# Kernel tuning notes

Measured on AMD Instinct MI355X. Metric: run time of the kernel, lower is better.

The kernel has to match this reference:

```python
import jax, jax.numpy as jnp
import numpy as np

N_NODES = 100000
N_EDGES = 1600000
D_IN, D_HID, D_OUT = 64, 128, 64


def setup_inputs() -> dict:
    key = jax.random.key(0)
    ks = jax.random.split(key, 12)
    s = lambda d: 1.0 / np.sqrt(d)
    return {
        "x": jax.random.normal(ks[0], (N_NODES, D_IN), dtype=jnp.float32),
        "edge_index": jax.random.randint(ks[1], (2, N_EDGES), 0, N_NODES, dtype=jnp.int64),
        # conv1 MLP: Linear(D_IN->D_HID), ReLU, Linear(D_HID->D_HID)
        "W1a": jax.random.uniform(ks[2], (D_IN, D_HID), jnp.float32, -s(D_IN), s(D_IN)),
        "b1a": jnp.zeros((D_HID,), jnp.float32),
        "W1b": jax.random.uniform(ks[3], (D_HID, D_HID), jnp.float32, -s(D_HID), s(D_HID)),
        "b1b": jnp.zeros((D_HID,), jnp.float32),
        # conv2 MLP: Linear(D_HID->D_HID), ReLU, Linear(D_HID->D_HID)
        "W2a": jax.random.uniform(ks[4], (D_HID, D_HID), jnp.float32, -s(D_HID), s(D_HID)),
        "b2a": jnp.zeros((D_HID,), jnp.float32),
        "W2b": jax.random.uniform(ks[5], (D_HID, D_HID), jnp.float32, -s(D_HID), s(D_HID)),
        "b2b": jnp.zeros((D_HID,), jnp.float32),
        # final projection Linear(D_HID->D_OUT)
        "Wlin": jax.random.uniform(ks[6], (D_HID, D_OUT), jnp.float32, -s(D_HID), s(D_HID)),
        "blin": jnp.zeros((D_OUT,), jnp.float32),
    }


def _gin_conv(h, src, dst, Wa, ba, Wb, bb, num_nodes):
    # GINConv (eps=0): MLP((1+eps)*x + sum_{j->i} x_j)
    agg = jax.ops.segment_sum(h[src], dst, num_segments=num_nodes)  # [N, d]
    z = h + agg
    z = jax.nn.relu(z @ Wa + ba)
    return z @ Wb + bb


def reference(x, edge_index, W1a, b1a, W1b, b1b, W2a, b2a, W2b, b2b, Wlin, blin):
    n = x.shape[0]
    src, dst = edge_index[0], edge_index[1]
    h = jax.nn.relu(_gin_conv(x, src, dst, W1a, b1a, W1b, b1b, n))
    h = jax.nn.relu(_gin_conv(h, src, dst, W2a, b2a, W2b, b2b, n))
    return h @ Wlin + blin  # [N, D_OUT]
```

## Files before the change

kernel.cpp:

```cpp
#include <hip/hip_runtime.h>
#include <hip/hip_fp16.h>


typedef __attribute__((ext_vector_type(8))) short short8;
typedef __attribute__((ext_vector_type(4))) float f32x4;
union F8 { unsigned u[4]; short8 s; };

__device__ inline unsigned bfpair(float v) {
    unsigned u = __float_as_uint(v);
    unsigned rh = u + 0x7fffu + ((u >> 16) & 1u);
    unsigned hf = rh & 0xffff0000u;
    float lof = v - __uint_as_float(hf);
    unsigned ul = __float_as_uint(lof);
    unsigned rl = ul + 0x7fffu + ((ul >> 16) & 1u);
    return (rh >> 16) | (rl & 0xffff0000u);
}


constexpr int BUCKET_SHIFT = 9;
constexpr int BUCKET_NODES = 1 << BUCKET_SHIFT;
constexpr int CAP = 10240;
constexpr int EPB = 4096;
constexpr int NBUCK_MAX = 256;

__global__ __launch_bounds__(256) void init_gcur_kernel(int* __restrict__ gcur, int nbuck) {
    int i = threadIdx.x;
    if (i < nbuck) gcur[i] = i * CAP;
}

__global__ __launch_bounds__(256) void bucket_scatter_kernel(const int* __restrict__ ei, int E,
                                                             int* __restrict__ gcur,
                                                             int* __restrict__ gpk,
                                                             int nbuck) {
    __shared__ int spk[EPB];
    __shared__ unsigned char sbuck[EPB];
    __shared__ int lcnt[NBUCK_MAX];
    __shared__ int lbase[NBUCK_MAX];
    __shared__ int lcur[NBUCK_MAX];
    __shared__ int gbase[NBUCK_MAX];
    __shared__ int stmp[256];

    const int t = threadIdx.x;
    const int e0 = blockIdx.x * EPB;
    const int ecnt = min(EPB, E - e0);

    for (int i = t; i < NBUCK_MAX; i += 256) lcnt[i] = 0;
    __syncthreads();

    for (int i = t; i < ecnt; i += 256) {
        int d = ei[E + e0 + i];
        atomicAdd(&lcnt[d >> BUCKET_SHIFT], 1);
    }
    __syncthreads();

    int v = lcnt[t];
    stmp[t] = v;
    __syncthreads();
    #pragma unroll
    for (int off = 1; off < 256; off <<= 1) {
        int add = (t >= off) ? stmp[t - off] : 0;
        __syncthreads();
        stmp[t] += add;
        __syncthreads();
    }
    lbase[t] = stmp[t] - v;
    lcur[t] = stmp[t] - v;
    __syncthreads();

    for (int i = t; i < ecnt; i += 256) {
        int s = ei[e0 + i];
        int d = ei[E + e0 + i];
        int b = d >> BUCKET_SHIFT;
        int p = atomicAdd(&lcur[b], 1);
        spk[p] = ((d & (BUCKET_NODES - 1)) << 17) | s;
        sbuck[p] = (unsigned char)b;
    }
    __syncthreads();

    if (t < nbuck) {
        int c = lcnt[t];
        gbase[t] = (c > 0) ? atomicAdd(&gcur[t], c) : 0;
    }
    __syncthreads();

    for (int i = t; i < ecnt; i += 256) {
        int b = sbuck[i];
        int gp = gbase[b] + (i - lbase[b]);
        if (gp < (b + 1) * CAP) gpk[gp] = spk[i];
    }
}

__global__ __launch_bounds__(256) void bucket_hist_kernel(const int* __restrict__ gpk,
                                                          const int* __restrict__ gcur,
                                                          int* __restrict__ cnt, int N) {
    __shared__ int h[BUCKET_NODES];
    const int t = threadIdx.x;
    const int b = blockIdx.x;
    const int base = b << BUCKET_SHIFT;
    for (int i = t; i < BUCKET_NODES; i += 256) h[i] = 0;
    __syncthreads();
    int cb = min(gcur[b] - b * CAP, CAP);
    const int* pp = gpk + (size_t)b * CAP;
    for (int i = t; i < cb; i += 256) atomicAdd(&h[((unsigned)pp[i]) >> 17], 1);
    __syncthreads();
    for (int i = t; i < BUCKET_NODES && base + i < N; i += 256) cnt[base + i] = h[i];
}

__global__ __launch_bounds__(256) void scan_block_kernel(const int* __restrict__ cnt,
                                                         int* __restrict__ rs,
                                                         int* __restrict__ partials,
                                                         int N) {
    __shared__ int s[256];
    int t = threadIdx.x;
    int i = blockIdx.x * 256 + t;
    int v = (i < N) ? cnt[i] : 0;
    s[t] = v;
    __syncthreads();
    #pragma unroll
    for (int off = 1; off < 256; off <<= 1) {
        int add = (t >= off) ? s[t - off] : 0;
        __syncthreads();
        s[t] += add;
        __syncthreads();
    }
    if (i < N) rs[i] = s[t] - v;
    if (t == 255) partials[blockIdx.x] = s[255];
}

__global__ __launch_bounds__(512) void scan_partials_kernel(int* __restrict__ partials,
                                                            int nb) {
    __shared__ int s[512];
    int t = threadIdx.x;
    int v = (t < nb) ? partials[t] : 0;
    s[t] = v;
    __syncthreads();
    #pragma unroll
    for (int off = 1; off < 512; off <<= 1) {
        int add = (t >= off) ? s[t - off] : 0;
        __syncthreads();
        s[t] += add;
        __syncthreads();
    }
    if (t < nb) partials[t] = s[t] - v;
}

__global__ __launch_bounds__(256) void scan_add_kernel(int* __restrict__ rs,
                                                       const int* __restrict__ partials,
                                                       int N, int E) {
    int i = blockIdx.x * 256 + threadIdx.x;
    if (i < N) rs[i] += partials[blockIdx.x];
    if (i == 0) rs[N] = E;
}

__global__ __launch_bounds__(256) void bucket_fill_kernel(const int* __restrict__ gpk,
                                                          const int* __restrict__ gcur,
                                                          const int* __restrict__ rs,
                                                          int* __restrict__ edge_src, int N) {
    __shared__ int cur[BUCKET_NODES];
    const int t = threadIdx.x;
    const int b = blockIdx.x;
    const int base = b << BUCKET_SHIFT;
    for (int i = t; i < BUCKET_NODES; i += 256) cur[i] = rs[min(base + i, N)];
    __syncthreads();
    int cb = min(gcur[b] - b * CAP, CAP);
    const int* pp = gpk + (size_t)b * CAP;
    for (int i = t; i < cb; i += 256) {
        unsigned pw = (unsigned)pp[i];
        int p = atomicAdd(&cur[pw >> 17], 1);
        edge_src[p] = (int)(pw & 0x1FFFFu);
    }
}


__global__ __launch_bounds__(256) void convert_fp16_kernel(const float* __restrict__ src,
                                                           __half2* __restrict__ dst, int n2) {
    int i = blockIdx.x * 256 + threadIdx.x;
    if (i < n2) {
        float2 v = reinterpret_cast<const float2*>(src)[i];
        dst[i] = __floats2half2_rn(v.x, v.y);
    }
}

__global__ __launch_bounds__(256) void agg128_fp16(const __half2* __restrict__ H16,
                                                   const int* __restrict__ row_start,
                                                   const int* __restrict__ edge_src,
                                                   __half2* __restrict__ Z16, int N) {
    int wave = threadIdx.x >> 6, lane = threadIdx.x & 63;
    int node = blockIdx.x * 4 + wave;
    if (node >= N) return;
    int beg = row_start[node], end = row_start[node + 1];
    float2 self = __half22float2(H16[(size_t)node * 64 + lane]);
    float a0 = self.x, a1 = self.y;
    int i = beg;
    for (; i + 4 <= end; i += 4) {
        int s0 = edge_src[i], s1 = edge_src[i + 1];
        int s2 = edge_src[i + 2], s3 = edge_src[i + 3];
        float2 v0 = __half22float2(H16[(size_t)s0 * 64 + lane]);
        float2 v1 = __half22float2(H16[(size_t)s1 * 64 + lane]);
        float2 v2 = __half22float2(H16[(size_t)s2 * 64 + lane]);
        float2 v3 = __half22float2(H16[(size_t)s3 * 64 + lane]);
        a0 += (v0.x + v1.x) + (v2.x + v3.x);
        a1 += (v0.y + v1.y) + (v2.y + v3.y);
    }
    for (; i < end; ++i) {
        float2 v = __half22float2(H16[(size_t)edge_src[i] * 64 + lane]);
        a0 += v.x;
        a1 += v.y;
    }
    Z16[(size_t)node * 64 + lane] = __floats2half2_rn(a0, a1);
}

__global__ __launch_bounds__(256) void agg64_fp16(const __half2* __restrict__ H16,
                                                  const int* __restrict__ row_start,
                                                  const int* __restrict__ edge_src,
                                                  __half2* __restrict__ Z16, int N) {
    int t = threadIdx.x;
    int grp = t >> 5;
    int gl = t & 31;
    int node = blockIdx.x * 8 + grp;
    if (node >= N) return;
    int beg = row_start[node], end = row_start[node + 1];
    float2 self = __half22float2(H16[(size_t)node * 32 + gl]);
    float a0 = self.x, a1 = self.y;
    int i = beg;
    for (; i + 4 <= end; i += 4) {
        int s0 = edge_src[i], s1 = edge_src[i + 1];
        int s2 = edge_src[i + 2], s3 = edge_src[i + 3];
        float2 v0 = __half22float2(H16[(size_t)s0 * 32 + gl]);
        float2 v1 = __half22float2(H16[(size_t)s1 * 32 + gl]);
        float2 v2 = __half22float2(H16[(size_t)s2 * 32 + gl]);
        float2 v3 = __half22float2(H16[(size_t)s3 * 32 + gl]);
        a0 += (v0.x + v1.x) + (v2.x + v3.x);
        a1 += (v0.y + v1.y) + (v2.y + v3.y);
    }
    for (; i < end; ++i) {
        float2 v = __half22float2(H16[(size_t)edge_src[i] * 32 + gl]);
        a0 += v.x;
        a1 += v.y;
    }
    Z16[(size_t)node * 32 + gl] = __floats2half2_rn(a0, a1);
}


__global__ __launch_bounds__(256) void prep_weights_kernel(const float* __restrict__ W1a,
                                                           const float* __restrict__ W1b,
                                                           const float* __restrict__ W2a,
                                                           const float* __restrict__ W2b,
                                                           const float* __restrict__ Wlin,
                                                           short* __restrict__ hi,
                                                           short* __restrict__ lo) {
    int i = blockIdx.x * 256 + threadIdx.x;
    const float* W;
    int base, K, N;
    if (i < 8192)       { W = W1a;  base = 0;     K = 64;  N = 128; }
    else if (i < 24576) { W = W1b;  base = 8192;  K = 128; N = 128; }
    else if (i < 40960) { W = W2a;  base = 24576; K = 128; N = 128; }
    else if (i < 57344) { W = W2b;  base = 40960; K = 128; N = 128; }
    else                { W = Wlin; base = 57344; K = 128; N = 64;  }
    int rel = i - base;
    int NT = N >> 4;
    int j  = rel & 7;
    int l  = (rel >> 3) & 63;
    int tc = rel >> 9;
    int nt = tc % NT;
    int c  = tc / NT;
    int n  = nt * 16 + (l & 15);
    int k  = c * 32 + ((l >> 4) << 3) + j;
    float v = W[k * N + n];
    unsigned p = bfpair(v);
    hi[i] = (short)(p & 0xffffu);
    lo[i] = (short)(p >> 16);
}


template <int K>
__device__ inline void stage_global16(const __half2* __restrict__ z, int M, int m0,
                                      unsigned* __restrict__ P, int t) {
    constexpr int KC = K / 32;
    constexpr int NF = 8 * KC * 64;
    #pragma unroll
    for (int fi = t; fi < NF; fi += 256) {
        int l = fi & 63;
        int tc = fi >> 6;
        int c = tc & (KC - 1);
        int T = tc / KC;
        int row = m0 + T * 16 + (l & 15);
        if (row >= M) row = M - 1;
        int kb = c * 32 + ((l >> 4) << 3);
        const __half2* p = z + (size_t)row * (K / 2) + (kb >> 1);
        uint4 v = *reinterpret_cast<const uint4*>(p);
        float2 f0 = __half22float2(*reinterpret_cast<__half2*>(&v.x));
        float2 f1 = __half22float2(*reinterpret_cast<__half2*>(&v.y));
        float2 f2 = __half22float2(*reinterpret_cast<__half2*>(&v.z));
        float2 f3 = __half22float2(*reinterpret_cast<__half2*>(&v.w));
        int base = ((T * KC + c) * 8) * 66 + l;
        P[base + 0 * 66] = bfpair(f0.x);
        P[base + 1 * 66] = bfpair(f0.y);
        P[base + 2 * 66] = bfpair(f1.x);
        P[base + 3 * 66] = bfpair(f1.y);
        P[base + 4 * 66] = bfpair(f2.x);
        P[base + 5 * 66] = bfpair(f2.y);
        P[base + 6 * 66] = bfpair(f3.x);
        P[base + 7 * 66] = bfpair(f3.y);
    }
}

template <int K, int NT>
__device__ inline void stage_compute(const unsigned* __restrict__ P,
                                     const short* __restrict__ WH,
                                     const short* __restrict__ WL,
                                     int w, int lane, f32x4 (*acc)[8]) {
    constexpr int KC = K / 32;
    const short8* bhp = reinterpret_cast<const short8*>(WH) + lane;
    const short8* blp = reinterpret_cast<const short8*>(WL) + lane;
    for (int c = 0; c < KC; ++c) {
        F8 bh[NT], bl[NT];
        #pragma unroll
        for (int nt = 0; nt < NT; ++nt) {
            bh[nt].s = bhp[(c * NT + nt) * 64];
            bl[nt].s = blp[(c * NT + nt) * 64];
        }
        #pragma unroll
        for (int mt = 0; mt < 2; ++mt) {
            const int T = w * 2 + mt;
            const unsigned* Pb = P + ((T * KC + c) * 8) * 66 + lane;
            unsigned d[8];
            #pragma unroll
            for (int j = 0; j < 8; ++j) d[j] = Pb[j * 66];
            F8 ah, al;
            #pragma unroll
            for (int j = 0; j < 4; ++j) {
                ah.u[j] = __builtin_amdgcn_perm(d[2 * j + 1], d[2 * j], 0x05040100u);
                al.u[j] = __builtin_amdgcn_perm(d[2 * j + 1], d[2 * j], 0x07060302u);
            }
            #pragma unroll
            for (int nt = 0; nt < NT; ++nt) {
                acc[mt][nt] = __builtin_amdgcn_mfma_f32_16x16x32_bf16(ah.s, bh[nt].s, acc[mt][nt], 0, 0, 0);
                acc[mt][nt] = __builtin_amdgcn_mfma_f32_16x16x32_bf16(al.s, bh[nt].s, acc[mt][nt], 0, 0, 0);
                acc[mt][nt] = __builtin_amdgcn_mfma_f32_16x16x32_bf16(ah.s, bl[nt].s, acc[mt][nt], 0, 0, 0);
            }
        }
    }
}

__device__ inline void epilogue_tile(const f32x4* acc, const float* __restrict__ bias,
                                     unsigned* __restrict__ Pout, int T, int lane) {
    int q = lane >> 4, ln = lane & 15;
    #pragma unroll
    for (int nt = 0; nt < 8; ++nt) {
        int col = nt * 16 + ln;
        float b = bias[col];
        int c = col >> 5, jj = col & 7, q2 = (col >> 3) & 3;
        int pb = ((T * 4 + c) * 8 + jj) * 66;
        #pragma unroll
        for (int r = 0; r < 4; ++r) {
            float v = fmaxf(acc[nt][r] + b, 0.f);
            Pout[pb + ((q * 4 + r) | (q2 << 4))] = bfpair(v);
        }
    }
}

__global__ __launch_bounds__(256, 2) void mfma_mlp_A(const __half2* __restrict__ z16,
                                                     const short* __restrict__ WaH,
                                                     const short* __restrict__ WaL,
                                                     const float* __restrict__ ba,
                                                     const short* __restrict__ WbH,
                                                     const short* __restrict__ WbL,
                                                     const float* __restrict__ bb,
                                                     __half* __restrict__ H16out, int M) {
    __shared__ unsigned P[8 * 4 * 8 * 66];
    const int t = threadIdx.x;
    const int w = t >> 6, lane = t & 63;
    const int m0 = blockIdx.x * 128;
    const int q = lane >> 4, ln = lane & 15;

    stage_global16<64>(z16, M, m0, P, t);
    __syncthreads();

    f32x4 acc[2][8];
    #pragma unroll
    for (int mt = 0; mt < 2; ++mt)
        #pragma unroll
        for (int i = 0; i < 8; ++i) acc[mt][i] = (f32x4){0.f, 0.f, 0.f, 0.f};
    stage_compute<64, 8>(P, WaH, WaL, w, lane, acc);
    __syncthreads();
    epilogue_tile(acc[0], ba, P, w * 2 + 0, lane);
    epilogue_tile(acc[1], ba, P, w * 2 + 1, lane);
    __syncthreads();

    #pragma unroll
    for (int mt = 0; mt < 2; ++mt)
        #pragma unroll
        for (int i = 0; i < 8; ++i) acc[mt][i] = (f32x4){0.f, 0.f, 0.f, 0.f};
    stage_compute<128, 8>(P, WbH, WbL, w, lane, acc);

    #pragma unroll
    for (int mt = 0; mt < 2; ++mt) {
        #pragma unroll
        for (int nt = 0; nt < 8; ++nt) {
            int col = nt * 16 + ln;
            float b = bb[col];
            #pragma unroll
            for (int r = 0; r < 4; ++r) {
                int row = m0 + (w * 2 + mt) * 16 + q * 4 + r;
                if (row < M) {
                    float v = fmaxf(acc[mt][nt][r] + b, 0.f);
                    H16out[(size_t)row * 128 + col] = __float2half_rn(v);
                }
            }
        }
    }
}

__global__ __launch_bounds__(256, 2) void mfma_mlp_B(const __half2* __restrict__ z16,
                                                     const short* __restrict__ WaH,
                                                     const short* __restrict__ WaL,
                                                     const float* __restrict__ ba,
                                                     const short* __restrict__ WbH,
                                                     const short* __restrict__ WbL,
                                                     const float* __restrict__ bb,
                                                     const short* __restrict__ WlH,
                                                     const short* __restrict__ WlL,
                                                     const float* __restrict__ bl,
                                                     float* __restrict__ Out, int M) {
    __shared__ unsigned P[8 * 4 * 8 * 66];
    const int t = threadIdx.x;
    const int w = t >> 6, lane = t & 63;
    const int m0 = blockIdx.x * 128;
    const int q = lane >> 4, ln = lane & 15;

    stage_global16<128>(z16, M, m0, P, t);
    __syncthreads();

    f32x4 acc[2][8];
    #pragma unroll
    for (int mt = 0; mt < 2; ++mt)
        #pragma unroll
        for (int i = 0; i < 8; ++i) acc[mt][i] = (f32x4){0.f, 0.f, 0.f, 0.f};
    stage_compute<128, 8>(P, WaH, WaL, w, lane, acc);
    __syncthreads();
    epilogue_tile(acc[0], ba, P, w * 2 + 0, lane);
    epilogue_tile(acc[1], ba, P, w * 2 + 1, lane);
    __syncthreads();

    #pragma unroll
    for (int mt = 0; mt < 2; ++mt)
        #pragma unroll
        for (int i = 0; i < 8; ++i) acc[mt][i] = (f32x4){0.f, 0.f, 0.f, 0.f};
    stage_compute<128, 8>(P, WbH, WbL, w, lane, acc);
    __syncthreads();
    epilogue_tile(acc[0], bb, P, w * 2 + 0, lane);
    epilogue_tile(acc[1], bb, P, w * 2 + 1, lane);
    __syncthreads();

    #pragma unroll
    for (int mt = 0; mt < 2; ++mt)
        #pragma unroll
        for (int i = 0; i < 8; ++i) acc[mt][i] = (f32x4){0.f, 0.f, 0.f, 0.f};
    stage_compute<128, 4>(P, WlH, WlL, w, lane, acc);

    #pragma unroll
    for (int mt = 0; mt < 2; ++mt) {
        #pragma unroll
        for (int nt = 0; nt < 4; ++nt) {
            int col = nt * 16 + ln;
            float b = bl[col];
            #pragma unroll
            for (int r = 0; r < 4; ++r) {
                int row = m0 + (w * 2 + mt) * 16 + q * 4 + r;
                if (row < M) Out[(size_t)row * 64 + col] = acc[mt][nt][r] + b;
            }
        }
    }
}


extern "C" void kernel_launch(void* const* d_in, const int* in_sizes, int n_in,
                              void* d_out, int out_size, void* d_ws, size_t ws_size,
                              hipStream_t stream) {
    const float* x    = (const float*)d_in[0];
    const int*   ei   = (const int*)d_in[1];
    const float* W1a  = (const float*)d_in[2];
    const float* b1a  = (const float*)d_in[3];
    const float* W1b  = (const float*)d_in[4];
    const float* b1b  = (const float*)d_in[5];
    const float* W2a  = (const float*)d_in[6];
    const float* b2a  = (const float*)d_in[7];
    const float* W2b  = (const float*)d_in[8];
    const float* b2b  = (const float*)d_in[9];
    const float* Wlin = (const float*)d_in[10];
    const float* blin = (const float*)d_in[11];
    float* out = (float*)d_out;

    const int N = in_sizes[0] / 64;
    const int E = in_sizes[1] / 2;
    const int NBUCK = (N + BUCKET_NODES - 1) >> BUCKET_SHIFT;

    char* ws = (char*)d_ws;
    const size_t bufBytes = (size_t)N * 128 * sizeof(float);
    __half2* Zbuf = (__half2*)(ws + 0);
    char* B = ws + bufBytes;
    size_t off = 3 * bufBytes;
    int* row_start = (int*)(ws + off); off += ((size_t)(N + 1) * 4 + 15) & ~(size_t)15;
    int* cnt       = (int*)(ws + off); off += ((size_t)N * 4 + 15) & ~(size_t)15;
    int* partials  = (int*)(ws + off); off += 4096;
    int* gcur      = (int*)(ws + off); off += 4096;
    int* edge_src  = (int*)(ws + off); off += (size_t)E * 4;
    __half* h116   = (__half*)(ws + off); off += (size_t)N * 128 * 2;
    int* gpk = (int*)B;
    short* wHi = (short*)(B + (32u << 20));
    short* wLo = wHi + 65536;
    __half* x16 = (__half*)(B + (36u << 20));
    short* w1aH = wHi + 0;     short* w1aL = wLo + 0;
    short* w1bH = wHi + 8192;  short* w1bL = wLo + 8192;
    short* w2aH = wHi + 24576; short* w2aL = wLo + 24576;
    short* w2bH = wHi + 40960; short* w2bL = wLo + 40960;
    short* wlH  = wHi + 57344; short* wlL  = wLo + 57344;

    const int NB_N = (N + 255) / 256;
    const int NB_G = (N + 127) / 128;
    const int NB_S = (E + EPB - 1) / EPB;
    const int NB_A128 = (N + 3) / 4;
    const int NB_A64  = (N + 7) / 8;
    const int NB_CVT  = (N * 64 / 2 + 255) / 256;

    prep_weights_kernel<<<256, 256, 0, stream>>>(W1a, W1b, W2a, W2b, Wlin, wHi, wLo);
    convert_fp16_kernel<<<NB_CVT, 256, 0, stream>>>(x, (__half2*)x16, N * 32);

    init_gcur_kernel<<<1, 256, 0, stream>>>(gcur, NBUCK);
    bucket_scatter_kernel<<<NB_S, 256, 0, stream>>>(ei, E, gcur, gpk, NBUCK);
    bucket_hist_kernel<<<NBUCK, 256, 0, stream>>>(gpk, gcur, cnt, N);
    scan_block_kernel<<<NB_N, 256, 0, stream>>>(cnt, row_start, partials, N);
    scan_partials_kernel<<<1, 512, 0, stream>>>(partials, NB_N);
    scan_add_kernel<<<NB_N, 256, 0, stream>>>(row_start, partials, N, E);
    bucket_fill_kernel<<<NBUCK, 256, 0, stream>>>(gpk, gcur, row_start, edge_src, N);

    agg64_fp16<<<NB_A64, 256, 0, stream>>>((const __half2*)x16, row_start, edge_src, Zbuf, N);
    mfma_mlp_A<<<NB_G, 256, 0, stream>>>(Zbuf, w1aH, w1aL, b1a, w1bH, w1bL, b1b, h116, N);

    agg128_fp16<<<NB_A128, 256, 0, stream>>>((const __half2*)h116, row_start, edge_src, Zbuf, N);
    mfma_mlp_B<<<NB_G, 256, 0, stream>>>(Zbuf, w2aH, w2aL, b2a, w2bH, w2bL, b2b,
                                         wlH, wlL, blin, out, N);
}
```

Baseline: 367.8 us.

## Split aggregation feature columns across blocks with 16-lane groups per node

Both neighbor-sum kernels now give each node a 16-lane group that covers only a quarter (128-wide) or half (64-wide) of the feature row. Adjacent blocks handle different column slices of the same 16 nodes. This puts more nodes in flight per wave to hide gather latency. In exchange, every column slice re-reads edge_src and row_start, and each gathered row segment is only 64 bytes, which may lower memory transaction efficiency.

```diff
diff --git a/kernel.cpp b/kernel.cpp
--- a/kernel.cpp
+++ b/kernel.cpp
@@ -181,64 +181,70 @@
     }
 }
 
-__global__ __launch_bounds__(256) void agg128_fp16(const __half2* __restrict__ H16,
-                                                   const int* __restrict__ row_start,
-                                                   const int* __restrict__ edge_src,
-                                                   __half2* __restrict__ Z16, int N) {
-    int wave = threadIdx.x >> 6, lane = threadIdx.x & 63;
-    int node = blockIdx.x * 4 + wave;
+__global__ __launch_bounds__(256) void agg128_fp16_q(const __half2* __restrict__ H16,
+                                                     const int* __restrict__ row_start,
+                                                     const int* __restrict__ edge_src,
+                                                     __half2* __restrict__ Z16, int N) {
+    int b = blockIdx.x;
+    int quarter = b & 3;
+    int grp = threadIdx.x >> 4;
+    int gl = threadIdx.x & 15;
+    int node = (b >> 2) * 16 + grp;
     if (node >= N) return;
+    int co = quarter * 16 + gl;
     int beg = row_start[node], end = row_start[node + 1];
-    float2 self = __half22float2(H16[(size_t)node * 64 + lane]);
+    float2 self = __half22float2(H16[(size_t)node * 64 + co]);
     float a0 = self.x, a1 = self.y;
     int i = beg;
     for (; i + 4 <= end; i += 4) {
         int s0 = edge_src[i], s1 = edge_src[i + 1];
         int s2 = edge_src[i + 2], s3 = edge_src[i + 3];
-        float2 v0 = __half22float2(H16[(size_t)s0 * 64 + lane]);
-        float2 v1 = __half22float2(H16[(size_t)s1 * 64 + lane]);
-        float2 v2 = __half22float2(H16[(size_t)s2 * 64 + lane]);
-        float2 v3 = __half22float2(H16[(size_t)s3 * 64 + lane]);
+        float2 v0 = __half22float2(H16[(size_t)s0 * 64 + co]);
+        float2 v1 = __half22float2(H16[(size_t)s1 * 64 + co]);
+        float2 v2 = __half22float2(H16[(size_t)s2 * 64 + co]);
+        float2 v3 = __half22float2(H16[(size_t)s3 * 64 + co]);
         a0 += (v0.x + v1.x) + (v2.x + v3.x);
         a1 += (v0.y + v1.y) + (v2.y + v3.y);
     }
     for (; i < end; ++i) {
-        float2 v = __half22float2(H16[(size_t)edge_src[i] * 64 + lane]);
+        float2 v = __half22float2(H16[(size_t)edge_src[i] * 64 + co]);
         a0 += v.x;
         a1 += v.y;
     }
-    Z16[(size_t)node * 64 + lane] = __floats2half2_rn(a0, a1);
-}
-
-__global__ __launch_bounds__(256) void agg64_fp16(const __half2* __restrict__ H16,
-                                                  const int* __restrict__ row_start,
-                                                  const int* __restrict__ edge_src,
-                                                  __half2* __restrict__ Z16, int N) {
-    int t = threadIdx.x;
-    int grp = t >> 5;
-    int gl = t & 31;
-    int node = blockIdx.x * 8 + grp;
+    Z16[(size_t)node * 64 + co] = __floats2half2_rn(a0, a1);
+}
+
+__global__ __launch_bounds__(256) void agg64_fp16_h(const __half2* __restrict__ H16,
+                                                    const int* __restrict__ row_start,
+                                                    const int* __restrict__ edge_src,
+                                                    __half2* __restrict__ Z16, int N) {
+    int b = blockIdx.x;
+    int half = b & 1;
+    int grp = threadIdx.x >> 4;
+    int gl = threadIdx.x & 15;
+    int node = (b >> 1) * 16 + grp;
     if (node >= N) return;
+    int co = half * 16 + gl;
     int beg = row_start[node], end = row_start[node + 1];
-    float2 self = __half22float2(H16[(size_t)node * 32 + gl]);
+    float2 self = __half22float2(H16[(size_t)node * 32 + co]);
     float a0 = self.x, a1 = self.y;
     int i = beg;
     for (; i + 4 <= end; i += 4) {
         int s0 = edge_src[i], s1 = edge_src[i + 1];
         int s2 = edge_src[i + 2], s3 = edge_src[i + 3];
-        float2 v0 = __half22float2(H16[(size_t)s0 * 32 + gl]);
-        float2 v1 = __half22float2(H16[(size_t)s1 * 32 + gl]);
-        float2 v2 = __half22float2(H16[(size_t)s2 * 32 + gl]);
-        float2 v3 = __half22float2(H16[(size_t)s3 * 32 + gl]);
+        float2 v0 = __half22float2(H16[(size_t)s0 * 32 + co]);
+        float2 v1 = __half22float2(H16[(size_t)s1 * 32 + co]);
+        float2 v2 = __half22float2(H16[(size_t)s2 * 32 + co]);
+        float2 v3 = __half22float2(H16[(size_t)s3 * 32 + co]);
         a0 += (v0.x + v1.x) + (v2.x + v3.x);
         a1 += (v0.y + v1.y) + (v2.y + v3.y);
     }
     for (; i < end; ++i) {
-        float2 v = __half22float2(H16[(size_t)edge_src[i] * 32 + gl]);
+        float2 v = __half22float2(H16[(size_t)edge_src[i] * 32 + co]);
         a0 += v.x;
         a1 += v.y;
     }
-    Z16[(size_t)node * 32 + gl] = __floats2half2_rn(a0, a1);
+    Z16[(size_t)node * 32 + co] = __floats2half2_rn(a0, a1);
 }
 
 
@@ -520,8 +526,8 @@
     const int NB_N = (N + 255) / 256;
     const int NB_G = (N + 127) / 128;
     const int NB_S = (E + EPB - 1) / EPB;
-    const int NB_A128 = (N + 3) / 4;
-    const int NB_A64  = (N + 7) / 8;
+    const int NB_A128 = 4 * ((N + 15) / 16);
+    const int NB_A64  = 2 * ((N + 15) / 16);
     const int NB_CVT  = (N * 64 / 2 + 255) / 256;
 
     prep_weights_kernel<<<256, 256, 0, stream>>>(W1a, W1b, W2a, W2b, Wlin, wHi, wLo);
@@ -535,10 +541,10 @@
     scan_add_kernel<<<NB_N, 256, 0, stream>>>(row_start, partials, N, E);
     bucket_fill_kernel<<<NBUCK, 256, 0, stream>>>(gpk, gcur, row_start, edge_src, N);
 
-    agg64_fp16<<<NB_A64, 256, 0, stream>>>((const __half2*)x16, row_start, edge_src, Zbuf, N);
+    agg64_fp16_h<<<NB_A64, 256, 0, stream>>>((const __half2*)x16, row_start, edge_src, Zbuf, N);
     mfma_mlp_A<<<NB_G, 256, 0, stream>>>(Zbuf, w1aH, w1aL, b1a, w1bH, w1bL, b1b, h116, N);
 
-    agg128_fp16<<<NB_A128, 256, 0, stream>>>((const __half2*)h116, row_start, edge_src, Zbuf, N);
+    agg128_fp16_q<<<NB_A128, 256, 0, stream>>>((const __half2*)h116, row_start, edge_src, Zbuf, N);
     mfma_mlp_B<<<NB_G, 256, 0, stream>>>(Zbuf, w2aH, w2aL, b2a, w2bH, w2bL, b2b,
                                          wlH, wlL, blin, out, N);
 }
```

Result: slower. 462.7 us (+25.8%).
